# Optimization experiments

Hardware: AMD Instinct MI355X
Metric: run time of the kernel (lower is better)

## Reference

```python
import jax, jax.numpy as jnp
import numpy as np
from jax import lax

FIR_TAPS = np.array([1.0, 3.0, 3.0, 1.0], dtype=np.float32)
FACTOR = 2
GAIN = 1.0


def _fir_kernel(C):
    # _setup_kernel: outer product, normalize to sum 1; upsample scales by gain*factor**2
    k = np.outer(FIR_TAPS, FIR_TAPS)
    k = k / k.sum() * (GAIN * FACTOR ** 2)  # 4x4 kernel, sum == 4
    k = jnp.asarray(k, jnp.float32)
    return jnp.tile(k[None, None], (C, 1, 1, 1))  # [C,1,4,4] depthwise


def setup_inputs() -> dict:
    key = jax.random.key(0)
    k1, k2, k3 = jax.random.split(key, 3)
    x = jax.random.normal(k1, (16, 256, 64, 64), jnp.float32)
    W = jax.random.normal(k2, (256, 256, 3, 3), jnp.float32) * 0.02
    b = jax.random.normal(k3, (256,), jnp.float32) * 0.02
    return {"x": x, "W": W, "b": b}


def reference(x, W, b):
    B, C, H, Wd = x.shape
    kern = _fir_kernel(C)
    # upfirdn2d upsample: zero-insert by 2 (lhs_dilation), pad0=2 / pad1=1(+up-1=2),
    # depthwise FIR correlation -> [B, C, 2H, 2W]
    p0, p1 = 2, 2  # pad1 = p//2 + (factor-1) trailing zeros folded into padding
    h = lax.conv_general_dilated(
        x, kern, window_strides=(1, 1), padding=((p0, p1), (p0, p1)),
        lhs_dilation=(FACTOR, FACTOR),
        dimension_numbers=("NCHW", "OIHW", "NCHW"), feature_group_count=C)
    # 3x3 conv, padding=1, stride=1 -> [B, out_ch, 2H, 2W]
    y = lax.conv_general_dilated(
        h, W, window_strides=(1, 1), padding=((1, 1), (1, 1)),
        dimension_numbers=("NCHW", "OIHW", "NCHW"))
    return y + b[None, :, None, None]
```

## Files before the change

### kernel.cpp

```cpp
#include <hip/hip_runtime.h>
#include <hip/hip_bf16.h>
#include <stdint.h>

typedef __attribute__((ext_vector_type(8))) short bf16x8;
typedef __attribute__((ext_vector_type(4))) float f32x4;

#define PH 130
#define NT 72

__device__ __forceinline__ short f2bf(float f) {
  uint32_t u = __builtin_bit_cast(uint32_t, f);
  u = (u + 0x7FFFu + ((u >> 16) & 1u)) >> 16;
  return (short)u;
}

__device__ __forceinline__ uint32_t pack2bf(float lo, float hi) {
  return ((uint32_t)(uint16_t)f2bf(hi) << 16) | (uint16_t)f2bf(lo);
}

__device__ __forceinline__ void gload16(const void* g, void* l) {
  __builtin_amdgcn_global_load_lds(
      (const __attribute__((address_space(1))) void*)g,
      (__attribute__((address_space(3))) void*)l, 16, 0, 0);
}

__global__ void wpack(const float* __restrict__ W, short* __restrict__ A) {
  int tid = blockIdx.x * 256 + threadIdx.x;
  if (tid >= 256 * 2304) return;
  int co = tid / 2304;
  int r  = tid - co * 2304;
  int tap = r >> 8, ci = r & 255;
  A[tid] = f2bf(W[((size_t)(co * 256 + ci)) * 9 + tap]);
}

__global__ void fir_up(const float* __restrict__ x, short* __restrict__ hT) {
  const int bt = blockIdx.x;
  const int b = bt / 65, t = bt - b * 65;
  const int ci0 = blockIdx.y << 6;
  const int tid = threadIdx.x;

  if (t == 64) {
    short* r0 = hT + ((size_t)(b * PH + 0) * PH) * 256 + ci0;
    short* r1 = hT + ((size_t)(b * PH + 129) * PH) * 256 + ci0;
    for (int idx = tid; idx < PH * 32; idx += 256) {
      int qp = idx >> 5, c2 = (idx & 31) * 2;
      *(uint32_t*)&r0[(size_t)qp * 256 + c2] = 0u;
      *(uint32_t*)&r1[(size_t)qp * 256 + c2] = 0u;
    }
    return;
  }

  __shared__ float F[2][64][65];
#pragma unroll
  for (int it = 0; it < 4; ++it) {
    int idx = it * 256 + tid;
    int ci = idx >> 4, jq = idx & 15;
    const float* base = &x[((size_t)(b * 256 + ci0 + ci) * 64) * 64 + jq * 4];
    f32x4 vm = {0.f, 0.f, 0.f, 0.f}, vp = {0.f, 0.f, 0.f, 0.f};
    f32x4 v0 = *(const f32x4*)(base + (size_t)t * 64);
    if (t >= 1)  vm = *(const f32x4*)(base + (size_t)(t - 1) * 64);
    if (t <= 62) vp = *(const f32x4*)(base + (size_t)(t + 1) * 64);
#pragma unroll
    for (int e = 0; e < 4; ++e) {
      F[0][jq * 4 + e][ci] = 0.25f * vm[e] + 0.75f * v0[e];
      F[1][jq * 4 + e][ci] = 0.75f * v0[e] + 0.25f * vp[e];
    }
  }
  __syncthreads();

  const int c2 = (tid & 31) * 2;
  const int qg = tid >> 5;
#pragma unroll
  for (int r = 0; r < 2; ++r) {
    short* outrow = hT + ((size_t)(b * PH + (2 * t + 1 + r)) * PH) * 256 + ci0;
    for (int qp = qg; qp < PH; qp += 8) {
      uint32_t out = 0u;
      if (qp >= 1 && qp <= 128) {
        int q = qp - 1;
        int par = q & 1;
        int jb = (q >> 1) - 1 + par;
        float wc0 = par ? 0.75f : 0.25f;
        float wc1 = par ? 0.25f : 0.75f;
        float v00 = 0.f, v01 = 0.f, v10 = 0.f, v11 = 0.f;
        if (jb >= 0)     { v00 = F[r][jb][c2];     v01 = F[r][jb][c2 + 1]; }
        if (jb + 1 < 64) { v10 = F[r][jb + 1][c2]; v11 = F[r][jb + 1][c2 + 1]; }
        out = pack2bf(wc0 * v00 + wc1 * v10, wc0 * v01 + wc1 * v11);
      }
      *(uint32_t*)&outrow[(size_t)qp * 256 + c2] = out;
    }
  }
}

__global__ __launch_bounds__(256, 3) void conv3x3_gemm(
    const short* __restrict__ hT, const short* __restrict__ Wp,
    const float* __restrict__ bias, float* __restrict__ y) {
  __shared__ short ldsA[3][4096];
  __shared__ short ldsB[3][4096];
  const int tid = threadIdx.x;
  const int lane = tid & 63, w = tid >> 6;
  const int wm = w >> 1, wn = w & 1;

  const int bid = blockIdx.x;
  const int tau = (bid & 7) * 512 + (bid >> 3);
  const int mt = tau >> 1, nh = tau & 1;
  const int b = mt >> 7, p = mt & 127;

  const short* srcA[2];
  const short* srcB[2];
#pragma unroll
  for (int i = 0; i < 2; ++i) {
    int o = i * 4096 + tid * 16;
    int L = o ^ (((o >> 7) & 3) << 4);
    int row = L >> 6, kk = (L & 63) >> 1;
    srcA[i] = hT + ((size_t)((b * PH + p) * PH + row)) * 256 + kk;
    srcB[i] = Wp + (size_t)(nh * 128 + row) * 2304 + kk;
  }

  auto offA = [&](int t) {
    int tap = t >> 3, ci0 = (t & 7) << 5;
    int dm = (tap >= 6) ? 2 : (tap >= 3) ? 1 : 0;
    int dn = tap - 3 * dm;
    return (dm * PH + dn) * 256 + ci0;
  };
  auto offB = [&](int t) { return (t >> 3) * 256 + ((t & 7) << 5); };

  auto stage = [&](int t) {
    int buf = t % 3;
    int oa = offA(t), ob = offB(t);
#pragma unroll
    for (int i = 0; i < 2; ++i) {
      gload16(srcA[i] + oa, &ldsA[buf][i * 2048] + (tid << 3));
      gload16(srcB[i] + ob, &ldsB[buf][i * 2048] + (tid << 3));
    }
  };

  const int aP = ((wm * 64 + (lane & 15)) * 64 + (lane >> 4) * 16)
                 ^ ((((lane & 15) >> 1) & 3) << 4);
  const int bP = ((wn * 64 + (lane & 15)) * 64 + (lane >> 4) * 16)
                 ^ ((((lane & 15) >> 1) & 3) << 4);

  f32x4 acc[4][4];
#pragma unroll
  for (int m = 0; m < 4; ++m)
#pragma unroll
    for (int n = 0; n < 4; ++n) acc[m][n] = (f32x4){0.f, 0.f, 0.f, 0.f};

  stage(0); stage(1);
  asm volatile("s_waitcnt vmcnt(4)" ::: "memory");
  __builtin_amdgcn_s_barrier();

  for (int t = 0; t < NT; ++t) {
    const char* LA = (const char*)&ldsA[t % 3][0];
    const char* LB = (const char*)&ldsB[t % 3][0];

    bf16x8 a_[4], b_[4];
#pragma unroll
    for (int m = 0; m < 4; ++m) a_[m] = *(const bf16x8*)(LA + aP + m * 1024);
#pragma unroll
    for (int n = 0; n < 4; ++n) b_[n] = *(const bf16x8*)(LB + bP + n * 1024);
    if (t + 2 < NT) stage(t + 2);
    asm volatile("s_waitcnt lgkmcnt(0)" ::: "memory");
    __builtin_amdgcn_s_setprio(1);
#pragma unroll
    for (int m = 0; m < 4; ++m)
#pragma unroll
      for (int n = 0; n < 4; ++n)
        acc[m][n] = __builtin_amdgcn_mfma_f32_16x16x32_bf16(a_[m], b_[n], acc[m][n], 0, 0, 0);
    __builtin_amdgcn_s_setprio(0);
    if (t < NT - 2)       asm volatile("s_waitcnt vmcnt(4)" ::: "memory");
    else if (t == NT - 2) asm volatile("s_waitcnt vmcnt(0)" ::: "memory");
    if (t < NT - 1) __builtin_amdgcn_s_barrier();
  }

#pragma unroll
  for (int n = 0; n < 4; ++n) {
    int co = nh * 128 + wn * 64 + n * 16 + (lane & 15);
    float bv = bias[co];
    float* yp = y + (((size_t)(b * 256 + co)) * 128 + p) * 128;
#pragma unroll
    for (int m = 0; m < 4; ++m) {
      int q0 = wm * 64 + m * 16 + ((lane >> 4) << 2);
      f32x4 vv = acc[m][n];
      vv[0] += bv; vv[1] += bv; vv[2] += bv; vv[3] += bv;
      *(f32x4*)(yp + q0) = vv;
    }
  }
}

extern "C" void kernel_launch(void* const* d_in, const int* in_sizes, int n_in,
                              void* d_out, int out_size, void* d_ws, size_t ws_size,
                              hipStream_t stream) {
  const float* x    = (const float*)d_in[0];
  const float* W    = (const float*)d_in[1];
  const float* bias = (const float*)d_in[2];
  float* y = (float*)d_out;

  const size_t hT_bytes = (size_t)16 * PH * PH * 256 * 2;
  const size_t A_bytes  = (size_t)256 * 2304 * 2;
  if (ws_size < hT_bytes + A_bytes) return;

  short* hT = (short*)d_ws;
  short* Wp = (short*)((char*)d_ws + hT_bytes);

  wpack<<<(256 * 2304 + 255) / 256, 256, 0, stream>>>(W, Wp);
  dim3 g1(16 * 65, 4);
  fir_up<<<g1, 256, 0, stream>>>(x, hT);
  conv3x3_gemm<<<4096, 256, 0, stream>>>(hT, Wp, bias, y);
}
```

Before: 444.8 us.

## Widen conv GEMM block tile to cover all 256 output channels

Each 512-thread block now computes a 128x256 output tile with 8 waves, so all output channels share one staged A (activation) tile. Previously two 256-thread blocks each staged the same A tile, so this halves A global loads and LDS fills. In exchange the B tile in LDS doubles, giving about 72KB of LDS per block. The tighter launch bounds (512, 4) may squeeze the register budget enough to cause spills or lower occupancy.

Result: faster. 402.2 us (-9.6%).

```diff
diff --git a/kernel.cpp b/kernel.cpp
--- a/kernel.cpp
+++ b/kernel.cpp
@@ -91,29 +91,33 @@
   }
 }
 
-__global__ __launch_bounds__(256, 3) void conv3x3_gemm(
+__global__ __launch_bounds__(512, 4) void conv3x3_gemm(
     const short* __restrict__ hT, const short* __restrict__ Wp,
     const float* __restrict__ bias, float* __restrict__ y) {
   __shared__ short ldsA[3][4096];
-  __shared__ short ldsB[3][4096];
+  __shared__ short ldsB[3][8192];
   const int tid = threadIdx.x;
   const int lane = tid & 63, w = tid >> 6;
-  const int wm = w >> 1, wn = w & 1;
+  const int wm = w >> 2, wn = w & 3;
 
   const int bid = blockIdx.x;
-  const int tau = (bid & 7) * 512 + (bid >> 3);
-  const int mt = tau >> 1, nh = tau & 1;
-  const int b = mt >> 7, p = mt & 127;
-
-  const short* srcA[2];
+  const int tau = (bid & 7) * 256 + (bid >> 3);
+  const int b = tau >> 7, p = tau & 127;
+
+  const short* srcA0;
   const short* srcB[2];
-#pragma unroll
-  for (int i = 0; i < 2; ++i) {
-    int o = i * 4096 + tid * 16;
+  {
+    int o = tid * 16;
     int L = o ^ (((o >> 7) & 3) << 4);
     int row = L >> 6, kk = (L & 63) >> 1;
-    srcA[i] = hT + ((size_t)((b * PH + p) * PH + row)) * 256 + kk;
-    srcB[i] = Wp + (size_t)(nh * 128 + row) * 2304 + kk;
+    srcA0 = hT + ((size_t)((b * PH + p) * PH + row)) * 256 + kk;
+  }
+#pragma unroll
+  for (int i = 0; i < 2; ++i) {
+    int o = i * 8192 + tid * 16;
+    int L = o ^ (((o >> 7) & 3) << 4);
+    int row = L >> 6, kk = (L & 63) >> 1;
+    srcB[i] = Wp + (size_t)row * 2304 + kk;
   }
 
   auto offA = [&](int t) {
@@ -127,17 +131,18 @@
   auto stage = [&](int t) {
     int buf = t % 3;
     int oa = offA(t), ob = offB(t);
-#pragma unroll
-    for (int i = 0; i < 2; ++i) {
-      gload16(srcA[i] + oa, &ldsA[buf][i * 2048] + (tid << 3));
-      gload16(srcB[i] + ob, &ldsB[buf][i * 2048] + (tid << 3));
-    }
+    gload16(srcA0 + oa, &ldsA[buf][0] + (tid << 3));
+    gload16(srcB[0] + ob, &ldsB[buf][0] + (tid << 3));
+    gload16(srcB[1] + ob, &ldsB[buf][4096] + (tid << 3));
   };
 
-  const int aP = ((wm * 64 + (lane & 15)) * 64 + (lane >> 4) * 16)
-                 ^ ((((lane & 15) >> 1) & 3) << 4);
-  const int bP = ((wn * 64 + (lane & 15)) * 64 + (lane >> 4) * 16)
-                 ^ ((((lane & 15) >> 1) & 3) << 4);
+  int aP, bP;
+  {
+    int La = (wm * 64 + (lane & 15)) * 64 + (lane >> 4) * 16;
+    aP = La ^ (((La >> 7) & 3) << 4);
+    int Lb = (wn * 64 + (lane & 15)) * 64 + (lane >> 4) * 16;
+    bP = Lb ^ (((Lb >> 7) & 3) << 4);
+  }
 
   f32x4 acc[4][4];
 #pragma unroll
@@ -146,7 +151,7 @@
     for (int n = 0; n < 4; ++n) acc[m][n] = (f32x4){0.f, 0.f, 0.f, 0.f};
 
   stage(0); stage(1);
-  asm volatile("s_waitcnt vmcnt(4)" ::: "memory");
+  asm volatile("s_waitcnt vmcnt(3)" ::: "memory");
   __builtin_amdgcn_s_barrier();
 
   for (int t = 0; t < NT; ++t) {
@@ -167,14 +172,14 @@
       for (int n = 0; n < 4; ++n)
         acc[m][n] = __builtin_amdgcn_mfma_f32_16x16x32_bf16(a_[m], b_[n], acc[m][n], 0, 0, 0);
     __builtin_amdgcn_s_setprio(0);
-    if (t < NT - 2)       asm volatile("s_waitcnt vmcnt(4)" ::: "memory");
+    if (t < NT - 2)       asm volatile("s_waitcnt vmcnt(3)" ::: "memory");
     else if (t == NT - 2) asm volatile("s_waitcnt vmcnt(0)" ::: "memory");
     if (t < NT - 1) __builtin_amdgcn_s_barrier();
   }
 
 #pragma unroll
   for (int n = 0; n < 4; ++n) {
-    int co = nh * 128 + wn * 64 + n * 16 + (lane & 15);
+    int co = wn * 64 + n * 16 + (lane & 15);
     float bv = bias[co];
     float* yp = y + (((size_t)(b * 256 + co)) * 128 + p) * 128;
 #pragma unroll
@@ -205,5 +210,5 @@
   wpack<<<(256 * 2304 + 255) / 256, 256, 0, stream>>>(W, Wp);
   dim3 g1(16 * 65, 4);
   fir_up<<<g1, 256, 0, stream>>>(x, hT);
-  conv3x3_gemm<<<4096, 256, 0, stream>>>(hT, Wp, bias, y);
-}
+  conv3x3_gemm<<<2048, 512, 0, stream>>>(hT, Wp, bias, y);
+}
```
